# Kernel tuning notes

Hardware: AMD Instinct MI355X
Metric: run time of the kernel (lower is better)

Reference implementation:

```python
import jax, jax.numpy as jnp
import numpy as np

NEURON_CDECAY = 0.5
NEURON_VDECAY = 0.75
NEURON_VTH = 0.5

B, D_IN, T = 4096, 1024, 16
H1, H2, D_OUT = 1024, 1024, 512


def setup_inputs() -> dict:
    key = jax.random.key(0)
    ks = jax.random.split(key, 7)
    def lin(k, fan_in, shape):
        bound = 1.0 / np.sqrt(fan_in)
        return jax.random.uniform(k, shape, jnp.float32, -bound, bound)
    # input spikes: binary-ish spike trains in [0,1)
    in_pop_spikes = (jax.random.uniform(ks[0], (B, D_IN, T)) < 0.3).astype(jnp.float32)
    return {
        "in_pop_spikes": in_pop_spikes,
        "W1": lin(ks[1], D_IN, (H1, D_IN)), "b1": lin(ks[2], D_IN, (H1,)),
        "W2": lin(ks[3], H1, (H2, H1)), "b2": lin(ks[4], H1, (H2,)),
        "Wo": lin(ks[5], H2, (D_OUT, H2)), "bo": lin(ks[6], H2, (D_OUT,)),
        "batch_size": B,
    }


def pseudo_spike(volt):
    return (volt > NEURON_VTH).astype(volt.dtype)


def clif_step(x, W, b, cur, volt, spk):
    cur = cur * NEURON_CDECAY + x @ W.T + b
    volt = volt * NEURON_VDECAY * (1.0 - spk) + cur
    spk = pseudo_spike(volt)
    return cur, volt, spk


def reference(in_pop_spikes, W1, b1, W2, b2, Wo, bo, batch_size):
    bsz = batch_size
    xs = jnp.transpose(in_pop_spikes, (2, 0, 1))  # [T, B, D_in]
    z = lambda d: jnp.zeros((bsz, d), jnp.float32)
    init = (z(H1), z(H1), z(H1), z(H2), z(H2), z(H2), z(D_OUT), z(D_OUT), z(D_OUT))

    def step(state, x):
        c1, v1, s1, c2, v2, s2, co, vo, so = state
        c1, v1, s1 = clif_step(x, W1, b1, c1, v1, s1)
        c2, v2, s2 = clif_step(s1, W2, b2, c2, v2, s2)
        co, vo, so = clif_step(s2, Wo, bo, co, vo, so)
        return (c1, v1, s1, c2, v2, s2, co, vo, so), so

    _, spikes = jax.lax.scan(step, init, xs)  # spikes: [T, B, D_out]
    return jnp.sum(spikes, axis=0) / T
```

## Files before the change

kernel.cpp:

```cpp
#include <hip/hip_runtime.h>


typedef __bf16 bf16x8_t __attribute__((ext_vector_type(8)));

static constexpr int BSZ   = 4096;
static constexpr int D_IN  = 1024;
static constexpr int H1    = 1024;
static constexpr int D_OUT = 512;
static constexpr int M_ROWS = BSZ * 16;

__global__ void pack_x(const float* __restrict__ X, __bf16* __restrict__ A) {
    const int P = blockIdx.x * 256 + threadIdx.x;
    const int b = P >> 10, d = P & 1023;
    const float4* xp = (const float4*)(X + (size_t)P * 16);
    float4 x0 = xp[0], x1 = xp[1], x2 = xp[2], x3 = xp[3];
    const float v[16] = {x0.x, x0.y, x0.z, x0.w, x1.x, x1.y, x1.z, x1.w,
                         x2.x, x2.y, x2.z, x2.w, x3.x, x3.y, x3.z, x3.w};
#pragma unroll
    for (int t = 0; t < 16; ++t)
        A[((size_t)(b * 16 + t)) * 1024 + d] = (__bf16)v[t];
}

__global__ __launch_bounds__(256) void gemm_np(
    const __bf16* __restrict__ A,
    const float* __restrict__ W,
    float* __restrict__ C,
    int N) {
#pragma clang fp contract(off)
    __shared__ float As[32][128];
    __shared__ float Ws[32][64];

    const int tid = threadIdx.x;
    const int tx = tid & 15;
    const int ty = tid >> 4;
    const int m0 = blockIdx.x * 128, n0 = blockIdx.y * 64;

    const int arow = tid & 127, akh = tid >> 7;
    const int wrow = tid & 63,  wks = tid >> 6;

    const __bf16* Ab = A + (size_t)(m0 + arow) * 1024 + akh * 16;
    const float*  Wb = W + (size_t)(n0 + wrow) * 1024 + wks * 8;

    float pacc[8][4] = {};

    for (int kt = 0; kt < 32; ++kt) {
        const int k0 = kt * 32;
        bf16x8_t av0 = *(const bf16x8_t*)(Ab + k0);
        bf16x8_t av1 = *(const bf16x8_t*)(Ab + k0 + 8);
        float4   wv0 = *(const float4*)(Wb + k0);
        float4   wv1 = *(const float4*)(Wb + k0 + 4);
        __syncthreads();
#pragma unroll
        for (int e = 0; e < 8; ++e) {
            As[akh * 16 + e][arow]     = (float)av0[e];
            As[akh * 16 + 8 + e][arow] = (float)av1[e];
        }
        Ws[wks * 8 + 0][wrow] = wv0.x;
        Ws[wks * 8 + 1][wrow] = wv0.y;
        Ws[wks * 8 + 2][wrow] = wv0.z;
        Ws[wks * 8 + 3][wrow] = wv0.w;
        Ws[wks * 8 + 4][wrow] = wv1.x;
        Ws[wks * 8 + 5][wrow] = wv1.y;
        Ws[wks * 8 + 6][wrow] = wv1.z;
        Ws[wks * 8 + 7][wrow] = wv1.w;
        __syncthreads();

#pragma unroll
        for (int kk = 0; kk < 32; ++kk) {
            float4 a0 = *(const float4*)&As[kk][ty * 8];
            float4 a1 = *(const float4*)&As[kk][ty * 8 + 4];
            float4 w  = *(const float4*)&Ws[kk][tx * 4];
            const float a[8] = {a0.x, a0.y, a0.z, a0.w, a1.x, a1.y, a1.z, a1.w};
            const float ww[4] = {w.x, w.y, w.z, w.w};
#pragma unroll
            for (int i = 0; i < 8; ++i)
#pragma unroll
                for (int j = 0; j < 4; ++j)
                    pacc[i][j] = __builtin_fmaf(a[i], ww[j], pacc[i][j]);
        }
    }

#pragma unroll
    for (int i = 0; i < 8; ++i) {
        float4 st = {pacc[i][0], pacc[i][1], pacc[i][2], pacc[i][3]};
        *(float4*)&C[(size_t)(m0 + ty * 8 + i) * N + (n0 + tx * 4)] = st;
    }
}

__global__ void recur_hidden(const float* __restrict__ Z, const float* __restrict__ bias,
                             __bf16* __restrict__ S) {
#pragma clang fp contract(off)
    const int idx = blockIdx.x * 256 + threadIdx.x;
    const int n = idx & 1023, b = idx >> 10;
    const float bb = bias[n];
    float c = 0.f, v = 0.f, s = 0.f;
#pragma unroll
    for (int t = 0; t < 16; ++t) {
        const float z = Z[(size_t)(b * 16 + t) * 1024 + n];
        const float t1 = c * 0.5f;
        const float t2 = t1 + z;
        c = t2 + bb;
        const float u1 = v * 0.75f;
        const float u2 = u1 * (1.0f - s);
        v = u2 + c;
        s = (v > 0.5f) ? 1.0f : 0.0f;
        S[(size_t)(b * 16 + t) * 1024 + n] = (__bf16)s;
    }
}

__global__ void recur_out(const float* __restrict__ Z, const float* __restrict__ bias,
                          float* __restrict__ Out) {
#pragma clang fp contract(off)
    const int idx = blockIdx.x * 256 + threadIdx.x;
    const int n = idx & 511, b = idx >> 9;
    const float bb = bias[n];
    float c = 0.f, v = 0.f, s = 0.f, acm = 0.f;
#pragma unroll
    for (int t = 0; t < 16; ++t) {
        const float z = Z[(size_t)(b * 16 + t) * 512 + n];
        const float t1 = c * 0.5f;
        const float t2 = t1 + z;
        c = t2 + bb;
        const float u1 = v * 0.75f;
        const float u2 = u1 * (1.0f - s);
        v = u2 + c;
        s = (v > 0.5f) ? 1.0f : 0.0f;
        acm += s;
    }
    Out[(size_t)b * 512 + n] = acm * 0.0625f;
}

extern "C" void kernel_launch(void* const* d_in, const int* in_sizes, int n_in,
                              void* d_out, int out_size, void* d_ws, size_t ws_size,
                              hipStream_t stream) {
    const float* X  = (const float*)d_in[0];
    const float* W1 = (const float*)d_in[1];
    const float* b1 = (const float*)d_in[2];
    const float* W2 = (const float*)d_in[3];
    const float* b2 = (const float*)d_in[4];
    const float* Wo = (const float*)d_in[5];
    const float* bo = (const float*)d_in[6];

    char* ws = (char*)d_ws;
    __bf16* A1 = (__bf16*)ws;
    __bf16* S1 = (__bf16*)(ws + (128ull << 20));
    float*  Z  = (float*)(ws + (256ull << 20));
    __bf16* S2 = A1;

    pack_x<<<(BSZ * D_IN) / 256, 256, 0, stream>>>(X, A1);

    gemm_np<<<dim3(M_ROWS / 128, H1 / 64), 256, 0, stream>>>(A1, W1, Z, H1);
    recur_hidden<<<(BSZ * H1) / 256, 256, 0, stream>>>(Z, b1, S1);
    gemm_np<<<dim3(M_ROWS / 128, H1 / 64), 256, 0, stream>>>(S1, W2, Z, H1);
    recur_hidden<<<(BSZ * H1) / 256, 256, 0, stream>>>(Z, b2, S2);
    gemm_np<<<dim3(M_ROWS / 128, D_OUT / 64), 256, 0, stream>>>(S2, Wo, Z, D_OUT);
    recur_out<<<(BSZ * D_OUT) / 256, 256, 0, stream>>>(Z, bo, (float*)d_out);
}
```

Baseline: 3.995 ms.

## Restructure FP32 GEMM to stream bf16 A from global with double-buffered W tile

Changes the GEMM tiling from 128x64 block tiles with both operands staged in LDS to 32x128 tiles. Each wave owns 8 rows and reads bf16 A directly from global memory as wave-uniform loads, unpacking the bf16 values with bit shifts. Only W is staged in LDS, double-buffered with a prefetch so there is one barrier per k-step. This removes the A-to-LDS transpose and one sync per iteration. In exchange each thread accumulates a smaller 8x2 tile, and W is re-read from L2 by four times as many blocks.

```diff
diff --git a/kernel.cpp b/kernel.cpp
--- a/kernel.cpp
+++ b/kernel.cpp
@@ -27,63 +27,84 @@
     float* __restrict__ C,
     int N) {
 #pragma clang fp contract(off)
-    __shared__ float As[32][128];
-    __shared__ float Ws[32][64];
+    __shared__ float Ws[2][32][128];
 
-    const int tid = threadIdx.x;
-    const int tx = tid & 15;
-    const int ty = tid >> 4;
-    const int m0 = blockIdx.x * 128, n0 = blockIdx.y * 64;
+    const int tid  = threadIdx.x;
+    const int lane = tid & 63;
+    const int wvu  = __builtin_amdgcn_readfirstlane(tid >> 6);
+    const int m0   = blockIdx.x * 32 + wvu * 8;
+    const int n0   = blockIdx.y * 128;
 
-    const int arow = tid & 127, akh = tid >> 7;
-    const int wrow = tid & 63,  wks = tid >> 6;
+    const int wrow = tid & 127, wks = tid >> 7;
+    const float* Wb = W + (size_t)(n0 + wrow) * 1024 + wks * 16;
 
-    const __bf16* Ab = A + (size_t)(m0 + arow) * 1024 + akh * 16;
-    const float*  Wb = W + (size_t)(n0 + wrow) * 1024 + wks * 8;
+    const char* Abase = (const char*)A + (size_t)m0 * 2048;
 
-    float pacc[8][4] = {};
+    float pacc[8][2] = {};
 
+    {
+        float4 wv0 = *(const float4*)(Wb);
+        float4 wv1 = *(const float4*)(Wb + 4);
+        float4 wv2 = *(const float4*)(Wb + 8);
+        float4 wv3 = *(const float4*)(Wb + 12);
+        const float wvv[16] = {wv0.x, wv0.y, wv0.z, wv0.w,
+                               wv1.x, wv1.y, wv1.z, wv1.w,
+                               wv2.x, wv2.y, wv2.z, wv2.w,
+                               wv3.x, wv3.y, wv3.z, wv3.w};
+#pragma unroll
+        for (int c = 0; c < 16; ++c)
+            Ws[0][wks * 16 + c][wrow] = wvv[c];
+    }
+    __syncthreads();
+
+    int cur = 0;
     for (int kt = 0; kt < 32; ++kt) {
-        const int k0 = kt * 32;
-        bf16x8_t av0 = *(const bf16x8_t*)(Ab + k0);
-        bf16x8_t av1 = *(const bf16x8_t*)(Ab + k0 + 8);
-        float4   wv0 = *(const float4*)(Wb + k0);
-        float4   wv1 = *(const float4*)(Wb + k0 + 4);
-        __syncthreads();
-#pragma unroll
-        for (int e = 0; e < 8; ++e) {
-            As[akh * 16 + e][arow]     = (float)av0[e];
-            As[akh * 16 + 8 + e][arow] = (float)av1[e];
-        }
-        Ws[wks * 8 + 0][wrow] = wv0.x;
-        Ws[wks * 8 + 1][wrow] = wv0.y;
-        Ws[wks * 8 + 2][wrow] = wv0.z;
-        Ws[wks * 8 + 3][wrow] = wv0.w;
-        Ws[wks * 8 + 4][wrow] = wv1.x;
-        Ws[wks * 8 + 5][wrow] = wv1.y;
-        Ws[wks * 8 + 6][wrow] = wv1.z;
-        Ws[wks * 8 + 7][wrow] = wv1.w;
-        __syncthreads();
+        const int ktn = (kt < 31) ? kt + 1 : 31;
+        float4 wv0 = *(const float4*)(Wb + ktn * 32);
+        float4 wv1 = *(const float4*)(Wb + ktn * 32 + 4);
+        float4 wv2 = *(const float4*)(Wb + ktn * 32 + 8);
+        float4 wv3 = *(const float4*)(Wb + ktn * 32 + 12);
 
 #pragma unroll
-        for (int kk = 0; kk < 32; ++kk) {
-            float4 a0 = *(const float4*)&As[kk][ty * 8];
-            float4 a1 = *(const float4*)&As[kk][ty * 8 + 4];
-            float4 w  = *(const float4*)&Ws[kk][tx * 4];
-            const float a[8] = {a0.x, a0.y, a0.z, a0.w, a1.x, a1.y, a1.z, a1.w};
-            const float ww[4] = {w.x, w.y, w.z, w.w};
+        for (int g = 0; g < 4; ++g) {
+            uint4 au[8];
 #pragma unroll
             for (int i = 0; i < 8; ++i)
+                au[i] = *(const uint4*)(Abase + (size_t)i * 2048 + kt * 64 + g * 16);
 #pragma unroll
-                for (int j = 0; j < 4; ++j)
-                    pacc[i][j] = __builtin_fmaf(a[i], ww[j], pacc[i][j]);
+            for (int k2 = 0; k2 < 8; ++k2) {
+                const int kk = g * 8 + k2;
+                float2 wv = *(const float2*)&Ws[cur][kk][lane * 2];
+#pragma unroll
+                for (int i = 0; i < 8; ++i) {
+                    const unsigned wrd = (k2 < 2) ? au[i].x
+                                       : (k2 < 4) ? au[i].y
+                                       : (k2 < 6) ? au[i].z : au[i].w;
+                    const unsigned bits = (k2 & 1) ? (wrd & 0xFFFF0000u)
+                                                   : (wrd << 16);
+                    const float ai = __builtin_bit_cast(float, bits);
+                    pacc[i][0] = __builtin_fmaf(ai, wv.x, pacc[i][0]);
+                    pacc[i][1] = __builtin_fmaf(ai, wv.y, pacc[i][1]);
+                }
+            }
         }
+
+        const int nxt = cur ^ 1;
+        const float wvv[16] = {wv0.x, wv0.y, wv0.z, wv0.w,
+                               wv1.x, wv1.y, wv1.z, wv1.w,
+                               wv2.x, wv2.y, wv2.z, wv2.w,
+                               wv3.x, wv3.y, wv3.z, wv3.w};
+#pragma unroll
+        for (int c = 0; c < 16; ++c)
+            Ws[nxt][wks * 16 + c][wrow] = wvv[c];
+        __syncthreads();
+        cur = nxt;
     }
 
 #pragma unroll
     for (int i = 0; i < 8; ++i) {
-        float4 st = {pacc[i][0], pacc[i][1], pacc[i][2], pacc[i][3]};
-        *(float4*)&C[(size_t)(m0 + ty * 8 + i) * N + (n0 + tx * 4)] = st;
+        float2 st = {pacc[i][0], pacc[i][1]};
+        *(float2*)&C[(size_t)(m0 + i) * N + n0 + lane * 2] = st;
     }
 }
 
@@ -149,10 +170,10 @@
 
     pack_x<<<(BSZ * D_IN) / 256, 256, 0, stream>>>(X, A1);
 
-    gemm_np<<<dim3(M_ROWS / 128, H1 / 64), 256, 0, stream>>>(A1, W1, Z, H1);
+    gemm_np<<<dim3(M_ROWS / 32, H1 / 128), 256, 0, stream>>>(A1, W1, Z, H1);
     recur_hidden<<<(BSZ * H1) / 256, 256, 0, stream>>>(Z, b1, S1);
-    gemm_np<<<dim3(M_ROWS / 128, H1 / 64), 256, 0, stream>>>(S1, W2, Z, H1);
+    gemm_np<<<dim3(M_ROWS / 32, H1 / 128), 256, 0, stream>>>(S1, W2, Z, H1);
     recur_hidden<<<(BSZ * H1) / 256, 256, 0, stream>>>(Z, b2, S2);
-    gemm_np<<<dim3(M_ROWS / 128, D_OUT / 64), 256, 0, stream>>>(S2, Wo, Z, D_OUT);
+    gemm_np<<<dim3(M_ROWS / 32, D_OUT / 128), 256, 0, stream>>>(S2, Wo, Z, D_OUT);
     recur_out<<<(BSZ * D_OUT) / 256, 256, 0, stream>>>(Z, bo, (float*)d_out);
 }
```

Result: slower. 11.49 ms (+187.5%).

## Replace LDS-tiled GEMM with register-blocked direct-load fp32 GEMM on pre-transposed weights

Applied to the files above, without the earlier changes.

Activations and spikes are now kept in fp32 instead of bf16. Weights are transposed into a scratch buffer, which reuses the output buffer. The GEMM drops shared-memory tiling: each thread loads its A rows and W^T columns straight from global memory, double-buffered in registers, and computes an 8x4 tile. The recurrence now overwrites Z in place. The aim is to remove LDS staging and barrier overhead, at the cost of twice the activation memory traffic and reliance on cache for operand reuse.

```diff
diff --git a/kernel.cpp b/kernel.cpp
--- a/kernel.cpp
+++ b/kernel.cpp
@@ -1,7 +1,7 @@
 #include <hip/hip_runtime.h>
 
 
-typedef __bf16 bf16x8_t __attribute__((ext_vector_type(8)));
+typedef float floatx4 __attribute__((ext_vector_type(4)));
 
 static constexpr int BSZ   = 4096;
 static constexpr int D_IN  = 1024;
@@ -9,7 +9,7 @@
 static constexpr int D_OUT = 512;
 static constexpr int M_ROWS = BSZ * 16;
 
-__global__ void pack_x(const float* __restrict__ X, __bf16* __restrict__ A) {
+__global__ void pack_x(const float* __restrict__ X, float* __restrict__ A) {
     const int P = blockIdx.x * 256 + threadIdx.x;
     const int b = P >> 10, d = P & 1023;
     const float4* xp = (const float4*)(X + (size_t)P * 16);
@@ -18,77 +18,72 @@
                          x2.x, x2.y, x2.z, x2.w, x3.x, x3.y, x3.z, x3.w};
 #pragma unroll
     for (int t = 0; t < 16; ++t)
-        A[((size_t)(b * 16 + t)) * 1024 + d] = (__bf16)v[t];
+        A[((size_t)(b * 16 + t)) * 1024 + d] = v[t];
+}
+
+__global__ void transp(const float* __restrict__ W, float* __restrict__ Wt,
+                       int R) {
+    const int P = blockIdx.x * 256 + threadIdx.x;
+    const int k = P & 1023, n = P >> 10;
+    Wt[(size_t)k * R + n] = W[P];
 }
 
 __global__ __launch_bounds__(256) void gemm_np(
-    const __bf16* __restrict__ A,
-    const float* __restrict__ W,
+    const float* __restrict__ A,
+    const float* __restrict__ Wt,
     float* __restrict__ C,
     int N) {
 #pragma clang fp contract(off)
-    __shared__ float As[32][128];
-    __shared__ float Ws[32][64];
+    const int lane = threadIdx.x & 63;
+    const int wv   = threadIdx.x >> 6;
+    const int m0   = blockIdx.x * 32 + wv * 8;
+    const int n0   = blockIdx.y * 256 + lane * 4;
 
-    const int tid = threadIdx.x;
-    const int tx = tid & 15;
-    const int ty = tid >> 4;
-    const int m0 = blockIdx.x * 128, n0 = blockIdx.y * 64;
+    const float* Ar = A + (size_t)m0 * 1024;
+    const float* Wr = Wt + n0;
 
-    const int arow = tid & 127, akh = tid >> 7;
-    const int wrow = tid & 63,  wks = tid >> 6;
+    float acc[8][4] = {};
+    floatx4 aA[8], aB[8], wA[4], wB[4];
 
-    const __bf16* Ab = A + (size_t)(m0 + arow) * 1024 + akh * 16;
-    const float*  Wb = W + (size_t)(n0 + wrow) * 1024 + wks * 8;
+#define LOADG(ab, wb, g) do {                                                  \
+    _Pragma("unroll")                                                          \
+    for (int i = 0; i < 8; ++i)                                                \
+        ab[i] = *(const floatx4*)(Ar + (size_t)i * 1024 + (g) * 4);            \
+    _Pragma("unroll")                                                          \
+    for (int kk = 0; kk < 4; ++kk)                                             \
+        wb[kk] = *(const floatx4*)(Wr + (size_t)((g) * 4 + kk) * N);           \
+} while (0)
 
-    float pacc[8][4] = {};
+#define COMPG(ab, wb) do {                                                     \
+    _Pragma("unroll")                                                          \
+    for (int kk = 0; kk < 4; ++kk)                                             \
+        _Pragma("unroll")                                                      \
+        for (int i = 0; i < 8; ++i)                                            \
+            _Pragma("unroll")                                                  \
+            for (int j = 0; j < 4; ++j)                                        \
+                acc[i][j] = __builtin_fmaf(ab[i][kk], wb[kk][j], acc[i][j]);   \
+} while (0)
 
-    for (int kt = 0; kt < 32; ++kt) {
-        const int k0 = kt * 32;
-        bf16x8_t av0 = *(const bf16x8_t*)(Ab + k0);
-        bf16x8_t av1 = *(const bf16x8_t*)(Ab + k0 + 8);
-        float4   wv0 = *(const float4*)(Wb + k0);
-        float4   wv1 = *(const float4*)(Wb + k0 + 4);
-        __syncthreads();
-#pragma unroll
-        for (int e = 0; e < 8; ++e) {
-            As[akh * 16 + e][arow]     = (float)av0[e];
-            As[akh * 16 + 8 + e][arow] = (float)av1[e];
-        }
-        Ws[wks * 8 + 0][wrow] = wv0.x;
-        Ws[wks * 8 + 1][wrow] = wv0.y;
-        Ws[wks * 8 + 2][wrow] = wv0.z;
-        Ws[wks * 8 + 3][wrow] = wv0.w;
-        Ws[wks * 8 + 4][wrow] = wv1.x;
-        Ws[wks * 8 + 5][wrow] = wv1.y;
-        Ws[wks * 8 + 6][wrow] = wv1.z;
-        Ws[wks * 8 + 7][wrow] = wv1.w;
-        __syncthreads();
-
-#pragma unroll
-        for (int kk = 0; kk < 32; ++kk) {
-            float4 a0 = *(const float4*)&As[kk][ty * 8];
-            float4 a1 = *(const float4*)&As[kk][ty * 8 + 4];
-            float4 w  = *(const float4*)&Ws[kk][tx * 4];
-            const float a[8] = {a0.x, a0.y, a0.z, a0.w, a1.x, a1.y, a1.z, a1.w};
-            const float ww[4] = {w.x, w.y, w.z, w.w};
-#pragma unroll
-            for (int i = 0; i < 8; ++i)
-#pragma unroll
-                for (int j = 0; j < 4; ++j)
-                    pacc[i][j] = __builtin_fmaf(a[i], ww[j], pacc[i][j]);
-        }
+    LOADG(aA, wA, 0);
+#pragma unroll 1
+    for (int g = 0; g < 256; g += 2) {
+        LOADG(aB, wB, g + 1);
+        COMPG(aA, wA);
+        const int gn = (g + 2 < 256) ? (g + 2) : 255;
+        LOADG(aA, wA, gn);
+        COMPG(aB, wB);
     }
+#undef LOADG
+#undef COMPG
 
 #pragma unroll
     for (int i = 0; i < 8; ++i) {
-        float4 st = {pacc[i][0], pacc[i][1], pacc[i][2], pacc[i][3]};
-        *(float4*)&C[(size_t)(m0 + ty * 8 + i) * N + (n0 + tx * 4)] = st;
+        floatx4 st = {acc[i][0], acc[i][1], acc[i][2], acc[i][3]};
+        *(floatx4*)&C[(size_t)(m0 + i) * N + n0] = st;
     }
 }
 
-__global__ void recur_hidden(const float* __restrict__ Z, const float* __restrict__ bias,
-                             __bf16* __restrict__ S) {
+__global__ void recur_hidden(float* __restrict__ Z, const float* __restrict__ bias) {
 #pragma clang fp contract(off)
     const int idx = blockIdx.x * 256 + threadIdx.x;
     const int n = idx & 1023, b = idx >> 10;
@@ -96,7 +91,8 @@
     float c = 0.f, v = 0.f, s = 0.f;
 #pragma unroll
     for (int t = 0; t < 16; ++t) {
-        const float z = Z[(size_t)(b * 16 + t) * 1024 + n];
+        const size_t p = (size_t)(b * 16 + t) * 1024 + n;
+        const float z = Z[p];
         const float t1 = c * 0.5f;
         const float t2 = t1 + z;
         c = t2 + bb;
@@ -104,7 +100,7 @@
         const float u2 = u1 * (1.0f - s);
         v = u2 + c;
         s = (v > 0.5f) ? 1.0f : 0.0f;
-        S[(size_t)(b * 16 + t) * 1024 + n] = (__bf16)s;
+        Z[p] = s;
     }
 }
 
@@ -142,17 +138,19 @@
     const float* bo = (const float*)d_in[6];
 
     char* ws = (char*)d_ws;
-    __bf16* A1 = (__bf16*)ws;
-    __bf16* S1 = (__bf16*)(ws + (128ull << 20));
-    float*  Z  = (float*)(ws + (256ull << 20));
-    __bf16* S2 = A1;
+    float* buf0 = (float*)ws;
+    float* buf1 = (float*)(ws + (256ull << 20));
+    float* WT   = (float*)d_out;
 
-    pack_x<<<(BSZ * D_IN) / 256, 256, 0, stream>>>(X, A1);
+    pack_x<<<(BSZ * D_IN) / 256, 256, 0, stream>>>(X, buf0);
 
-    gemm_np<<<dim3(M_ROWS / 128, H1 / 64), 256, 0, stream>>>(A1, W1, Z, H1);
-    recur_hidden<<<(BSZ * H1) / 256, 256, 0, stream>>>(Z, b1, S1);
-    gemm_np<<<dim3(M_ROWS / 128, H1 / 64), 256, 0, stream>>>(S1, W2, Z, H1);
-    recur_hidden<<<(BSZ * H1) / 256, 256, 0, stream>>>(Z, b2, S2);
-    gemm_np<<<dim3(M_ROWS / 128, D_OUT / 64), 256, 0, stream>>>(S2, Wo, Z, D_OUT);
-    recur_out<<<(BSZ * D_OUT) / 256, 256, 0, stream>>>(Z, bo, (float*)d_out);
+    transp<<<(H1 * 1024) / 256, 256, 0, stream>>>(W1, WT, H1);
+    gemm_np<<<dim3(M_ROWS / 32, H1 / 256), 256, 0, stream>>>(buf0, WT, buf1, H1);
+    recur_hidden<<<(BSZ * H1) / 256, 256, 0, stream>>>(buf1, b1);
+    transp<<<(H1 * 1024) / 256, 256, 0, stream>>>(W2, WT, H1);
+    gemm_np<<<dim3(M_ROWS / 32, H1 / 256), 256, 0, stream>>>(buf1, WT, buf0, H1);
+    recur_hidden<<<(BSZ * H1) / 256, 256, 0, stream>>>(buf0, b2);
+    transp<<<(D_OUT * 1024) / 256, 256, 0, stream>>>(Wo, WT, D_OUT);
+    gemm_np<<<dim3(M_ROWS / 32, D_OUT / 256), 256, 0, stream>>>(buf0, WT, buf1, D_OUT);
+    recur_out<<<(BSZ * D_OUT) / 256, 256, 0, stream>>>(buf1, bo, (float*)d_out);
 }
```

New measurement: 8.144 ms. 104% more time.
